# Kernel tuning notes

Measured on AMD Instinct MI355X. Metric: run time of the kernel, lower is better.

The kernel has to match this reference:

```python
import jax, jax.numpy as jnp
import numpy as np

N_NODES = 50000
N_EDGES = 800000
IN_CH = 128
HID = 128
LAT = 64


def setup_inputs() -> dict:
    key = jax.random.key(0)
    ks = jax.random.split(key, 8)
    s = 1.0 / np.sqrt(IN_CH)
    sh = 1.0 / np.sqrt(HID)
    x = jax.random.normal(ks[0], (N_NODES, IN_CH), dtype=jnp.float32)
    edge_index = jax.random.randint(ks[1], (2, N_EDGES), 0, N_NODES, dtype=jnp.int64)
    return {
        "x": x,
        "edge_index": edge_index,
        "W1": jax.random.normal(ks[2], (IN_CH, HID), dtype=jnp.float32) * s,
        "b1": jnp.zeros((HID,), dtype=jnp.float32),
        "W2": jax.random.normal(ks[3], (HID, HID), dtype=jnp.float32) * sh,
        "b2": jnp.zeros((HID,), dtype=jnp.float32),
        "W_mu": jax.random.normal(ks[4], (HID, LAT), dtype=jnp.float32) * sh,
        "b_mu": jnp.zeros((LAT,), dtype=jnp.float32),
        "W_lv": jax.random.normal(ks[5], (HID, LAT), dtype=jnp.float32) * sh,
        "b_lv": jnp.zeros((LAT,), dtype=jnp.float32),
    }


def _gcn_norm(edge_index, num_nodes):
    # PyG gcn_norm with add_self_loops=True: deg[i] = in-degree(i) + 1
    src, dst = edge_index[0], edge_index[1]
    deg = jax.ops.segment_sum(jnp.ones((edge_index.shape[1],), jnp.float32), dst,
                              num_segments=num_nodes) + 1.0
    dinv = 1.0 / jnp.sqrt(deg)  # deg >= 1, never inf
    edge_norm = dinv[src] * dinv[dst]          # [E]
    self_norm = dinv * dinv                    # [N] norm for self-loop edges
    return src, dst, edge_norm, self_norm


def _gcn_conv(x, W, b, src, dst, edge_norm, self_norm, num_nodes):
    h = x @ W                                           # [N, out]
    msg = h[src] * edge_norm[:, None]                   # [E, out] gather
    agg = jax.ops.segment_sum(msg, dst, num_segments=num_nodes)  # scatter-add
    agg = agg + h * self_norm[:, None]                  # self-loop contribution
    return agg + b


def reference(x, edge_index, W1, b1, W2, b2, W_mu, b_mu, W_lv, b_lv):
    n = x.shape[0]
    src, dst, e_norm, s_norm = _gcn_norm(edge_index, n)
    h = jax.nn.relu(_gcn_conv(x, W1, b1, src, dst, e_norm, s_norm, n))
    h = jax.nn.relu(_gcn_conv(h, W2, b2, src, dst, e_norm, s_norm, n))
    mu = h @ W_mu + b_mu
    logvar = h @ W_lv + b_lv
    return mu, logvar
```

## Files before the change

### kernel.cpp

```cpp
#include <hip/hip_runtime.h>

#define NN 50000
#define NE 800000
#define BKT 64

typedef short s8v  __attribute__((ext_vector_type(8)));
typedef float f4v  __attribute__((ext_vector_type(4)));

__device__ __forceinline__ unsigned f2bf(float f) {
    unsigned u = __float_as_uint(f);
    return (u + 0x7fffu + ((u >> 16) & 1u)) >> 16;
}
__device__ __forceinline__ float bf2f_lo(unsigned u) { return __uint_as_float(u << 16); }
__device__ __forceinline__ float bf2f_hi(unsigned u) { return __uint_as_float(u & 0xffff0000u); }

__device__ __forceinline__ s8v pack8(float4 p, float4 q) {
    union { unsigned u[4]; s8v v; } r;
    r.u[0] = (f2bf(p.y) << 16) | f2bf(p.x);
    r.u[1] = (f2bf(p.w) << 16) | f2bf(p.z);
    r.u[2] = (f2bf(q.y) << 16) | f2bf(q.x);
    r.u[3] = (f2bf(q.w) << 16) | f2bf(q.z);
    return r.v;
}

__global__ __launch_bounds__(256) void k_prep(const float* __restrict__ W1, const float* __restrict__ W2,
                                              const float* __restrict__ Wmu, const float* __restrict__ Wlv,
                                              unsigned short* __restrict__ Wt, int* __restrict__ cursor) {
    int b = blockIdx.x;
    if (b < 192) {
        int idx = b * 256 + threadIdx.x;
        int m = idx >> 14, i = idx & 16383;
        int n = i & 127, k = i >> 7;
        float v;
        if (m == 0)      v = W1[k * 128 + n];
        else if (m == 1) v = W2[k * 128 + n];
        else             v = (n < 64) ? Wmu[k * 64 + n] : Wlv[k * 64 + (n - 64)];
        Wt[m * 16384 + n * 128 + k] = (unsigned short)f2bf(v);
    } else {
        int i = (b - 192) * 256 + threadIdx.x;
        if (i < NN) cursor[i] = 0;
    }
}

__global__ __launch_bounds__(256) void k_fg(const float4* __restrict__ x4,
                                            const unsigned short* __restrict__ Wt,
                                            unsigned short* __restrict__ Hb,
                                            const int* __restrict__ src, const int* __restrict__ dst,
                                            int* __restrict__ cursor, int* __restrict__ esrc) {
    int b = blockIdx.x;
    if (b % 9 != 8) {
        int fb = b - b / 9;
        int xcd = fb & 7;
        int idx = (fb >> 3) * 256 + (int)threadIdx.x;
        if (idx >= NE / 4) return;
        int4 d4 = ((const int4*)dst)[idx];
        int4 s4 = ((const int4*)src)[idx];
        int dv[4] = { d4.x, d4.y, d4.z, d4.w };
        int sv[4] = { s4.x, s4.y, s4.z, s4.w };
#pragma unroll
        for (int k = 0; k < 4; ++k) {
            int d = dv[k];
            if (d / (NN / 8) == xcd) {
                int p = atomicAdd(&cursor[d], 1);
                if (p < BKT) esrc[(size_t)d * BKT + p] = sv[k];
            }
        }
    } else {
        int bg = b / 9;
        int wave = threadIdx.x >> 6, lane = threadIdx.x & 63;
        int quad = lane >> 4, l16 = lane & 15;
        int row0 = bg * 64 + wave * 16;
        int arow = row0 + l16;
        int arc  = arow < NN ? arow : NN - 1;

        const float4* xq = x4 + (size_t)arc * 32;
        s8v a0 = pack8(xq[ 0 + quad * 2], xq[ 1 + quad * 2]);
        s8v a1 = pack8(xq[ 8 + quad * 2], xq[ 9 + quad * 2]);
        s8v a2 = pack8(xq[16 + quad * 2], xq[17 + quad * 2]);
        s8v a3 = pack8(xq[24 + quad * 2], xq[25 + quad * 2]);

        f4v acc[8];
#pragma unroll
        for (int c = 0; c < 8; ++c) acc[c] = (f4v)0.f;

#pragma unroll
        for (int c = 0; c < 8; ++c) {
            const s8v* wp = (const s8v*)(Wt + (size_t)(c * 16 + l16) * 128);
            acc[c] = __builtin_amdgcn_mfma_f32_16x16x32_bf16(a0, wp[quad],      acc[c], 0, 0, 0);
            acc[c] = __builtin_amdgcn_mfma_f32_16x16x32_bf16(a1, wp[4 + quad],  acc[c], 0, 0, 0);
            acc[c] = __builtin_amdgcn_mfma_f32_16x16x32_bf16(a2, wp[8 + quad],  acc[c], 0, 0, 0);
            acc[c] = __builtin_amdgcn_mfma_f32_16x16x32_bf16(a3, wp[12 + quad], acc[c], 0, 0, 0);
        }

#pragma unroll
        for (int c = 0; c < 8; ++c) {
#pragma unroll
            for (int r = 0; r < 4; ++r) {
                int ro = row0 + quad * 4 + r;
                if (ro < NN) Hb[(size_t)ro * 128 + c * 16 + l16] = (unsigned short)f2bf(acc[c][r]);
            }
        }
    }
}

#define ACCUM(K) { float lo = bf2f_lo(u[K]), hi = bf2f_hi(u[K]);            \
    switch ((K) & 3) {                                                       \
        case 0: ax0 += lo * w[K]; ay0 += hi * w[K]; break;                   \
        case 1: ax1 += lo * w[K]; ay1 += hi * w[K]; break;                   \
        case 2: ax2 += lo * w[K]; ay2 += hi * w[K]; break;                   \
        default: ax3 += lo * w[K]; ay3 += hi * w[K]; break; } }

__device__ __forceinline__ float2 agg_node(const unsigned* __restrict__ h2,
                                           const int* __restrict__ degc,
                                           const int* __restrict__ esrc,
                                           const float* __restrict__ b,
                                           int n, int lane) {
    int d = __builtin_amdgcn_readfirstlane(degc[n]);
    float dn = rsqrtf((float)(d + 1));
    int svr = esrc[(size_t)n * BKT + lane];
    unsigned suv = ((unsigned)svr < (unsigned)NN) ? (unsigned)svr : 0u;
    int dgv = degc[suv];
    float wsv = rsqrtf((float)(dgv + 1)) * dn;

    float ax0 = 0.f, ay0 = 0.f, ax1 = 0.f, ay1 = 0.f;
    float ax2 = 0.f, ay2 = 0.f, ax3 = 0.f, ay3 = 0.f;

    if (d <= 16) {
        unsigned u[16];
        float    w[16];
#pragma unroll
        for (int k = 0; k < 16; ++k) {
            unsigned su = (unsigned)__builtin_amdgcn_readlane((int)suv, k);
            float wk = __int_as_float(__builtin_amdgcn_readlane(__float_as_int(wsv), k));
            w[k] = (k < d) ? wk : 0.f;
            u[k] = h2[(size_t)su * 64 + lane];
        }
#pragma unroll
        for (int k = 0; k < 16; ++k) ACCUM(k)
    } else {
        unsigned u[24];
        float    w[24];
#pragma unroll
        for (int k = 0; k < 24; ++k) {
            unsigned su = (unsigned)__builtin_amdgcn_readlane((int)suv, k);
            float wk = __int_as_float(__builtin_amdgcn_readlane(__float_as_int(wsv), k));
            w[k] = (k < d) ? wk : 0.f;
            u[k] = h2[(size_t)su * 64 + lane];
        }
#pragma unroll
        for (int k = 0; k < 24; ++k) ACCUM(k)

        for (int e0 = 24; e0 < d; e0 += 8) {
            unsigned u[8];
            float    w[8];
#pragma unroll
            for (int k = 0; k < 8; ++k) {
                int ek  = e0 + k;
                int ekc = ek < (BKT - 1) ? ek : (BKT - 1);
                unsigned su = (unsigned)__builtin_amdgcn_readlane((int)suv, ekc);
                float wk = __int_as_float(__builtin_amdgcn_readlane(__float_as_int(wsv), ekc));
                w[k] = (ek < d) ? wk : 0.f;
                u[k] = h2[(size_t)su * 64 + lane];
            }
#pragma unroll
            for (int k = 0; k < 8; ++k) ACCUM(k)
        }
    }

    float sn = dn * dn;
    unsigned uh = h2[(size_t)n * 64 + lane];
    float2 bb = ((const float2*)b)[lane];
    float2 r;
    r.x = fmaxf((ax0 + ax1) + (ax2 + ax3) + bf2f_lo(uh) * sn + bb.x, 0.f);
    r.y = fmaxf((ay0 + ay1) + (ay2 + ay3) + bf2f_hi(uh) * sn + bb.y, 0.f);
    return r;
}

__global__ __launch_bounds__(512, 4) void k_ag8(const unsigned short* __restrict__ Hb_,
                                                const int* __restrict__ degc, const int* __restrict__ esrc,
                                                const float* __restrict__ b1,
                                                const unsigned short* __restrict__ Wt,
                                                unsigned short* __restrict__ Cb) {
    __shared__ __align__(16) unsigned lds[8][64];
    int w = threadIdx.x >> 6, lane = threadIdx.x & 63;
    int n = blockIdx.x * 8 + w;
    const unsigned* h2 = (const unsigned*)Hb_;

    float2 r = agg_node(h2, degc, esrc, b1, n, lane);
    lds[w][lane ^ (w << 2)] = (f2bf(r.y) << 16) | f2bf(r.x);
    __syncthreads();

    int quad = lane >> 4, l16 = lane & 15, kx = l16 & 7;
    const unsigned* rowp = &lds[l16 & 7][0];
    s8v a0 = *(const s8v*)(rowp + (( 0 + quad) ^ kx) * 4);
    s8v a1 = *(const s8v*)(rowp + (( 4 + quad) ^ kx) * 4);
    s8v a2 = *(const s8v*)(rowp + (( 8 + quad) ^ kx) * 4);
    s8v a3 = *(const s8v*)(rowp + ((12 + quad) ^ kx) * 4);
    if (l16 >= 8) { a0 = (s8v)0; a1 = (s8v)0; a2 = (s8v)0; a3 = (s8v)0; }

    const s8v* wp = (const s8v*)(Wt + (size_t)(w * 16 + l16) * 128);
    f4v acc = (f4v)0.f;
    acc = __builtin_amdgcn_mfma_f32_16x16x32_bf16(a0, wp[quad],      acc, 0, 0, 0);
    acc = __builtin_amdgcn_mfma_f32_16x16x32_bf16(a1, wp[4 + quad],  acc, 0, 0, 0);
    acc = __builtin_amdgcn_mfma_f32_16x16x32_bf16(a2, wp[8 + quad],  acc, 0, 0, 0);
    acc = __builtin_amdgcn_mfma_f32_16x16x32_bf16(a3, wp[12 + quad], acc, 0, 0, 0);

    int row0 = blockIdx.x * 8;
#pragma unroll
    for (int r2 = 0; r2 < 4; ++r2) {
        int ro8 = quad * 4 + r2;
        if (ro8 < 8)
            Cb[(size_t)(row0 + ro8) * 128 + w * 16 + l16] = (unsigned short)f2bf(acc[r2]);
    }
}

__global__ __launch_bounds__(512, 4) void k_af8(const unsigned short* __restrict__ Hb_,
                                                const int* __restrict__ degc, const int* __restrict__ esrc,
                                                const float* __restrict__ b2,
                                                const unsigned short* __restrict__ Wt,
                                                const float* __restrict__ bmu, const float* __restrict__ blv,
                                                float* __restrict__ out) {
    __shared__ __align__(16) unsigned lds[8][64];
    int w = threadIdx.x >> 6, lane = threadIdx.x & 63;
    int n = blockIdx.x * 8 + w;
    const unsigned* h2 = (const unsigned*)Hb_;

    float2 r = agg_node(h2, degc, esrc, b2, n, lane);
    lds[w][lane ^ (w << 2)] = (f2bf(r.y) << 16) | f2bf(r.x);
    __syncthreads();

    int quad = lane >> 4, l16 = lane & 15, kx = l16 & 7;
    const unsigned* rowp = &lds[l16 & 7][0];
    s8v a0 = *(const s8v*)(rowp + (( 0 + quad) ^ kx) * 4);
    s8v a1 = *(const s8v*)(rowp + (( 4 + quad) ^ kx) * 4);
    s8v a2 = *(const s8v*)(rowp + (( 8 + quad) ^ kx) * 4);
    s8v a3 = *(const s8v*)(rowp + ((12 + quad) ^ kx) * 4);
    if (l16 >= 8) { a0 = (s8v)0; a1 = (s8v)0; a2 = (s8v)0; a3 = (s8v)0; }

    const s8v* wp = (const s8v*)(Wt + (size_t)(w * 16 + l16) * 128);
    f4v acc = (f4v)0.f;
    acc = __builtin_amdgcn_mfma_f32_16x16x32_bf16(a0, wp[quad],      acc, 0, 0, 0);
    acc = __builtin_amdgcn_mfma_f32_16x16x32_bf16(a1, wp[4 + quad],  acc, 0, 0, 0);
    acc = __builtin_amdgcn_mfma_f32_16x16x32_bf16(a2, wp[8 + quad],  acc, 0, 0, 0);
    acc = __builtin_amdgcn_mfma_f32_16x16x32_bf16(a3, wp[12 + quad], acc, 0, 0, 0);

    int row0 = blockIdx.x * 8;
    int col  = w * 16 + l16;
    float bb = (col < 64) ? bmu[col] : blv[col - 64];
#pragma unroll
    for (int r2 = 0; r2 < 4; ++r2) {
        int ro8 = quad * 4 + r2;
        if (ro8 < 8) {
            int ro = row0 + ro8;
            float v = acc[r2] + bb;
            if (col < 64) out[(size_t)ro * 64 + col] = v;
            else          out[(size_t)NN * 64 + (size_t)ro * 64 + (col - 64)] = v;
        }
    }
}

extern "C" void kernel_launch(void* const* d_in, const int* in_sizes, int n_in,
                              void* d_out, int out_size, void* d_ws, size_t ws_size,
                              hipStream_t stream) {
    const float* x    = (const float*)d_in[0];
    const int*   eidx = (const int*)d_in[1];
    const float* W1   = (const float*)d_in[2];
    const float* b1   = (const float*)d_in[3];
    const float* W2   = (const float*)d_in[4];
    const float* b2   = (const float*)d_in[5];
    const float* Wmu  = (const float*)d_in[6];
    const float* bmu  = (const float*)d_in[7];
    const float* Wlv  = (const float*)d_in[8];
    const float* blv  = (const float*)d_in[9];
    float* out = (float*)d_out;

    const int* src = eidx;
    const int* dst = eidx + NE;

    float*          ws     = (float*)d_ws;
    int*            cursor = (int*)ws;
    int*            esrc   = (int*)(ws + 50048);
    unsigned short* Wt     = (unsigned short*)(ws + 3250048);
    unsigned short* Hb     = (unsigned short*)(ws + 3274624);
    unsigned short* Hb2    = (unsigned short*)(ws + 6474624);

    const int gFG = 7038;
    const int gA  = 6250;

    k_prep<<<388, 256, 0, stream>>>(W1, W2, Wmu, Wlv, Wt, cursor);

    k_fg<<<gFG, 256, 0, stream>>>((const float4*)x, Wt, Hb, src, dst, cursor, esrc);

    k_ag8<<<gA, 512, 0, stream>>>(Hb, cursor, esrc, b1, Wt + 16384, Hb2);

    k_af8<<<gA, 512, 0, stream>>>(Hb2, cursor, esrc, b2, Wt + 32768, bmu, blv, out);
}
```

Baseline: 238.6 us.

## Drop weight-prep kernel; build bf16 weight fragments from fp32 weights inline

Removes the k_prep launch. Each consumer kernel now reads the fp32 weights directly and converts them to bf16 MFMA fragments in registers, and the cursor is zeroed with hipMemsetAsync. The per-node bucket capacity BKT drops from 64 to 48, which shrinks the esrc workspace and moves the other buffers closer together. The trade is more strided scalar global loads and conversions in every block, which matters most in k_fg where they sit inside the MFMA loop. Nodes with more than 48 in-edges could also overflow a bucket if nothing else handles them.

```diff
diff --git a/kernel.cpp b/kernel.cpp
--- a/kernel.cpp
+++ b/kernel.cpp
@@ -2,7 +2,7 @@
 
 #define NN 50000
 #define NE 800000
-#define BKT 64
+#define BKT 48
 
 typedef short s8v  __attribute__((ext_vector_type(8)));
 typedef float f4v  __attribute__((ext_vector_type(4)));
@@ -23,27 +23,17 @@
     return r.v;
 }
 
-__global__ __launch_bounds__(256) void k_prep(const float* __restrict__ W1, const float* __restrict__ W2,
-                                              const float* __restrict__ Wmu, const float* __restrict__ Wlv,
-                                              unsigned short* __restrict__ Wt, int* __restrict__ cursor) {
-    int b = blockIdx.x;
-    if (b < 192) {
-        int idx = b * 256 + threadIdx.x;
-        int m = idx >> 14, i = idx & 16383;
-        int n = i & 127, k = i >> 7;
-        float v;
-        if (m == 0)      v = W1[k * 128 + n];
-        else if (m == 1) v = W2[k * 128 + n];
-        else             v = (n < 64) ? Wmu[k * 64 + n] : Wlv[k * 64 + (n - 64)];
-        Wt[m * 16384 + n * 128 + k] = (unsigned short)f2bf(v);
-    } else {
-        int i = (b - 192) * 256 + threadIdx.x;
-        if (i < NN) cursor[i] = 0;
-    }
+__device__ __forceinline__ s8v wfrag(const float* __restrict__ W, int ldw, int n, int kc) {
+    const float* p = W + (size_t)kc * 8 * ldw + n;
+    union { unsigned u[4]; s8v v; } r;
+#pragma unroll
+    for (int t = 0; t < 4; ++t)
+        r.u[t] = (f2bf(p[(size_t)(2 * t + 1) * ldw]) << 16) | f2bf(p[(size_t)(2 * t) * ldw]);
+    return r.v;
 }
 
 __global__ __launch_bounds__(256) void k_fg(const float4* __restrict__ x4,
-                                            const unsigned short* __restrict__ Wt,
+                                            const float* __restrict__ W1,
                                             unsigned short* __restrict__ Hb,
                                             const int* __restrict__ src, const int* __restrict__ dst,
                                             int* __restrict__ cursor, int* __restrict__ esrc) {
@@ -85,11 +75,15 @@
 
 #pragma unroll
         for (int c = 0; c < 8; ++c) {
-            const s8v* wp = (const s8v*)(Wt + (size_t)(c * 16 + l16) * 128);
-            acc[c] = __builtin_amdgcn_mfma_f32_16x16x32_bf16(a0, wp[quad],      acc[c], 0, 0, 0);
-            acc[c] = __builtin_amdgcn_mfma_f32_16x16x32_bf16(a1, wp[4 + quad],  acc[c], 0, 0, 0);
-            acc[c] = __builtin_amdgcn_mfma_f32_16x16x32_bf16(a2, wp[8 + quad],  acc[c], 0, 0, 0);
-            acc[c] = __builtin_amdgcn_mfma_f32_16x16x32_bf16(a3, wp[12 + quad], acc[c], 0, 0, 0);
+            int n = c * 16 + l16;
+            s8v w0 = wfrag(W1, 128, n, quad);
+            s8v w1 = wfrag(W1, 128, n, 4 + quad);
+            s8v w2 = wfrag(W1, 128, n, 8 + quad);
+            s8v w3 = wfrag(W1, 128, n, 12 + quad);
+            acc[c] = __builtin_amdgcn_mfma_f32_16x16x32_bf16(a0, w0, acc[c], 0, 0, 0);
+            acc[c] = __builtin_amdgcn_mfma_f32_16x16x32_bf16(a1, w1, acc[c], 0, 0, 0);
+            acc[c] = __builtin_amdgcn_mfma_f32_16x16x32_bf16(a2, w2, acc[c], 0, 0, 0);
+            acc[c] = __builtin_amdgcn_mfma_f32_16x16x32_bf16(a3, w3, acc[c], 0, 0, 0);
         }
 
 #pragma unroll
@@ -179,18 +173,24 @@
 __global__ __launch_bounds__(512, 4) void k_ag8(const unsigned short* __restrict__ Hb_,
                                                 const int* __restrict__ degc, const int* __restrict__ esrc,
                                                 const float* __restrict__ b1,
-                                                const unsigned short* __restrict__ Wt,
+                                                const float* __restrict__ W2,
                                                 unsigned short* __restrict__ Cb) {
     __shared__ __align__(16) unsigned lds[8][64];
     int w = threadIdx.x >> 6, lane = threadIdx.x & 63;
+    int quad = lane >> 4, l16 = lane & 15;
     int n = blockIdx.x * 8 + w;
     const unsigned* h2 = (const unsigned*)Hb_;
+
+    s8v w0 = wfrag(W2, 128, w * 16 + l16, quad);
+    s8v w1 = wfrag(W2, 128, w * 16 + l16, 4 + quad);
+    s8v w2 = wfrag(W2, 128, w * 16 + l16, 8 + quad);
+    s8v w3 = wfrag(W2, 128, w * 16 + l16, 12 + quad);
 
     float2 r = agg_node(h2, degc, esrc, b1, n, lane);
     lds[w][lane ^ (w << 2)] = (f2bf(r.y) << 16) | f2bf(r.x);
     __syncthreads();
 
-    int quad = lane >> 4, l16 = lane & 15, kx = l16 & 7;
+    int kx = l16 & 7;
     const unsigned* rowp = &lds[l16 & 7][0];
     s8v a0 = *(const s8v*)(rowp + (( 0 + quad) ^ kx) * 4);
     s8v a1 = *(const s8v*)(rowp + (( 4 + quad) ^ kx) * 4);
@@ -198,12 +198,11 @@
     s8v a3 = *(const s8v*)(rowp + ((12 + quad) ^ kx) * 4);
     if (l16 >= 8) { a0 = (s8v)0; a1 = (s8v)0; a2 = (s8v)0; a3 = (s8v)0; }
 
-    const s8v* wp = (const s8v*)(Wt + (size_t)(w * 16 + l16) * 128);
     f4v acc = (f4v)0.f;
-    acc = __builtin_amdgcn_mfma_f32_16x16x32_bf16(a0, wp[quad],      acc, 0, 0, 0);
-    acc = __builtin_amdgcn_mfma_f32_16x16x32_bf16(a1, wp[4 + quad],  acc, 0, 0, 0);
-    acc = __builtin_amdgcn_mfma_f32_16x16x32_bf16(a2, wp[8 + quad],  acc, 0, 0, 0);
-    acc = __builtin_amdgcn_mfma_f32_16x16x32_bf16(a3, wp[12 + quad], acc, 0, 0, 0);
+    acc = __builtin_amdgcn_mfma_f32_16x16x32_bf16(a0, w0, acc, 0, 0, 0);
+    acc = __builtin_amdgcn_mfma_f32_16x16x32_bf16(a1, w1, acc, 0, 0, 0);
+    acc = __builtin_amdgcn_mfma_f32_16x16x32_bf16(a2, w2, acc, 0, 0, 0);
+    acc = __builtin_amdgcn_mfma_f32_16x16x32_bf16(a3, w3, acc, 0, 0, 0);
 
     int row0 = blockIdx.x * 8;
 #pragma unroll
@@ -217,19 +216,27 @@
 __global__ __launch_bounds__(512, 4) void k_af8(const unsigned short* __restrict__ Hb_,
                                                 const int* __restrict__ degc, const int* __restrict__ esrc,
                                                 const float* __restrict__ b2,
-                                                const unsigned short* __restrict__ Wt,
+                                                const float* __restrict__ Wmu, const float* __restrict__ Wlv,
                                                 const float* __restrict__ bmu, const float* __restrict__ blv,
                                                 float* __restrict__ out) {
     __shared__ __align__(16) unsigned lds[8][64];
     int w = threadIdx.x >> 6, lane = threadIdx.x & 63;
+    int quad = lane >> 4, l16 = lane & 15;
     int n = blockIdx.x * 8 + w;
     const unsigned* h2 = (const unsigned*)Hb_;
+
+    int col = w * 16 + l16;
+    const float* Wp = (col < 64) ? (Wmu + col) : (Wlv + col - 64);
+    s8v w0 = wfrag(Wp, 64, 0, quad);
+    s8v w1 = wfrag(Wp, 64, 0, 4 + quad);
+    s8v w2 = wfrag(Wp, 64, 0, 8 + quad);
+    s8v w3 = wfrag(Wp, 64, 0, 12 + quad);
 
     float2 r = agg_node(h2, degc, esrc, b2, n, lane);
     lds[w][lane ^ (w << 2)] = (f2bf(r.y) << 16) | f2bf(r.x);
     __syncthreads();
 
-    int quad = lane >> 4, l16 = lane & 15, kx = l16 & 7;
+    int kx = l16 & 7;
     const unsigned* rowp = &lds[l16 & 7][0];
     s8v a0 = *(const s8v*)(rowp + (( 0 + quad) ^ kx) * 4);
     s8v a1 = *(const s8v*)(rowp + (( 4 + quad) ^ kx) * 4);
@@ -237,15 +244,13 @@
     s8v a3 = *(const s8v*)(rowp + ((12 + quad) ^ kx) * 4);
     if (l16 >= 8) { a0 = (s8v)0; a1 = (s8v)0; a2 = (s8v)0; a3 = (s8v)0; }
 
-    const s8v* wp = (const s8v*)(Wt + (size_t)(w * 16 + l16) * 128);
     f4v acc = (f4v)0.f;
-    acc = __builtin_amdgcn_mfma_f32_16x16x32_bf16(a0, wp[quad],      acc, 0, 0, 0);
-    acc = __builtin_amdgcn_mfma_f32_16x16x32_bf16(a1, wp[4 + quad],  acc, 0, 0, 0);
-    acc = __builtin_amdgcn_mfma_f32_16x16x32_bf16(a2, wp[8 + quad],  acc, 0, 0, 0);
-    acc = __builtin_amdgcn_mfma_f32_16x16x32_bf16(a3, wp[12 + quad], acc, 0, 0, 0);
+    acc = __builtin_amdgcn_mfma_f32_16x16x32_bf16(a0, w0, acc, 0, 0, 0);
+    acc = __builtin_amdgcn_mfma_f32_16x16x32_bf16(a1, w1, acc, 0, 0, 0);
+    acc = __builtin_amdgcn_mfma_f32_16x16x32_bf16(a2, w2, acc, 0, 0, 0);
+    acc = __builtin_amdgcn_mfma_f32_16x16x32_bf16(a3, w3, acc, 0, 0, 0);
 
     int row0 = blockIdx.x * 8;
-    int col  = w * 16 + l16;
     float bb = (col < 64) ? bmu[col] : blv[col - 64];
 #pragma unroll
     for (int r2 = 0; r2 < 4; ++r2) {
@@ -280,18 +285,17 @@
     float*          ws     = (float*)d_ws;
     int*            cursor = (int*)ws;
     int*            esrc   = (int*)(ws + 50048);
-    unsigned short* Wt     = (unsigned short*)(ws + 3250048);
-    unsigned short* Hb     = (unsigned short*)(ws + 3274624);
-    unsigned short* Hb2    = (unsigned short*)(ws + 6474624);
+    unsigned short* Hb     = (unsigned short*)(ws + 2450176);
+    unsigned short* Hb2    = (unsigned short*)(ws + 5650176);
 
     const int gFG = 7038;
     const int gA  = 6250;
 
-    k_prep<<<388, 256, 0, stream>>>(W1, W2, Wmu, Wlv, Wt, cursor);
-
-    k_fg<<<gFG, 256, 0, stream>>>((const float4*)x, Wt, Hb, src, dst, cursor, esrc);
-
-    k_ag8<<<gA, 512, 0, stream>>>(Hb, cursor, esrc, b1, Wt + 16384, Hb2);
-
-    k_af8<<<gA, 512, 0, stream>>>(Hb2, cursor, esrc, b2, Wt + 32768, bmu, blv, out);
-}
+    hipMemsetAsync(cursor, 0, 50048 * sizeof(int), stream);
+
+    k_fg<<<gFG, 256, 0, stream>>>((const float4*)x, W1, Hb, src, dst, cursor, esrc);
+
+    k_ag8<<<gA, 512, 0, stream>>>(Hb, cursor, esrc, b1, W2, Hb2);
+
+    k_af8<<<gA, 512, 0, stream>>>(Hb2, cursor, esrc, b2, Wmu, Wlv, bmu, blv, out);
+}
```

Measured after the change: 248.4 us. 1.04x slower.
